# Kernel optimization log

Hardware: AMD Instinct MI355X
Metric: run time of the kernel (lower is better)

Reference implementation:

```python
import jax, jax.numpy as jnp
import numpy as np

N, K, D, H, DK, DV, L, E = 16384, 16, 128, 8, 16, 16, 2, 32
DFF = 4 * D
EPS = 1e-5


def _ln(x, g, b):
    mu = jnp.mean(x, axis=-1, keepdims=True)
    var = jnp.var(x, axis=-1, keepdims=True)
    return (x - mu) * jax.lax.rsqrt(var + EPS) * g + b


def setup_inputs() -> dict:
    key = jax.random.key(0)
    ks = jax.random.split(key, 20)
    inp = {
        "node_h": jax.random.normal(ks[0], (N, D), jnp.float32),
        "src_idx": jax.random.randint(ks[1], (N, K), 0, N),
        "edge_feat": jax.random.normal(ks[2], (N, K, E), jnp.float32),
        "t": jax.random.uniform(ks[3], (N, K), jnp.float32),
        "t_now": jnp.ones((1,), jnp.float32),
        # params (linear weights stored [in, out])
        "edge_fc_w": jax.random.normal(ks[4], (E, D), jnp.float32) * (2.0 / (E + D)) ** 0.5,
        "edge_fc_b": jnp.zeros((D,), jnp.float32),
        "basis_freq": jnp.asarray(1.0 / 10 ** np.linspace(0, 9, D), jnp.float32),
        "phase": jax.random.normal(ks[5], (D,), jnp.float32),
        "wq": jax.random.normal(ks[6], (L, D, H * DK), jnp.float32) * np.sqrt(2.0 / (D + DK)),
        "wk": jax.random.normal(ks[7], (L, D, H * DK), jnp.float32) * np.sqrt(2.0 / (D + DK)),
        "wv": jax.random.normal(ks[8], (L, D, H * DV), jnp.float32) * np.sqrt(2.0 / (D + DV)),
        "attn_fc_w": jax.random.normal(ks[9], (L, H * DV, D), jnp.float32) * (2.0 / (H * DV + D)) ** 0.5,
        "attn_fc_b": jnp.zeros((L, D), jnp.float32),
        "attn_ln_g": jnp.ones((L, D), jnp.float32),
        "attn_ln_b": jnp.zeros((L, D), jnp.float32),
        "ffn_w1": jax.random.normal(ks[10], (L, D, DFF), jnp.float32) * (1.0 / D) ** 0.5,
        "ffn_b1": jnp.zeros((L, DFF), jnp.float32),
        "ffn_w2": jax.random.normal(ks[11], (L, DFF, D), jnp.float32) * (1.0 / DFF) ** 0.5,
        "ffn_b2": jnp.zeros((L, D), jnp.float32),
        "ffn_ln_g": jnp.ones((L, D), jnp.float32),
        "ffn_ln_b": jnp.zeros((L, D), jnp.float32),
        "fea2node_w": jax.random.normal(ks[12], (D, D), jnp.float32) * (2.0 / (D + D)) ** 0.5,
        "fea2node_b": jnp.zeros((D,), jnp.float32),
        "final_ln_g": jnp.ones((D,), jnp.float32),
        "final_ln_b": jnp.zeros((D,), jnp.float32),
    }
    return inp


def reference(node_h, src_idx, edge_feat, t, t_now,
              edge_fc_w, edge_fc_b, basis_freq, phase,
              wq, wk, wv, attn_fc_w, attn_fc_b, attn_ln_g, attn_ln_b,
              ffn_w1, ffn_b1, ffn_w2, ffn_b2, ffn_ln_g, ffn_ln_b,
              fea2node_w, fea2node_b, final_ln_g, final_ln_b):
    scale = 1.0 / np.sqrt(DK).astype(np.float32)
    # message_func: gather src features, edge transform, temporal encoding
    t_enc = jnp.cos((t_now[0] - t)[..., None] * basis_freq + phase)        # [N,K,D]
    z = node_h[src_idx] + jax.nn.gelu(edge_feat @ edge_fc_w + edge_fc_b) + t_enc
    # reduce_func: inner_layer transformer blocks over the K-neighbor mailbox
    f = z
    for i in range(L):
        q = (f @ wq[i]).reshape(N, K, H, DK)
        k = (f @ wk[i]).reshape(N, K, H, DK)
        v = (f @ wv[i]).reshape(N, K, H, DV)
        attn = jax.nn.softmax(jnp.einsum('nqhd,nkhd->nhqk', q, k) * scale, axis=-1)
        out = jnp.einsum('nhqk,nkhd->nqhd', attn, v).reshape(N, K, H * DV)
        f = _ln(out @ attn_fc_w[i] + attn_fc_b[i] + f, attn_ln_g[i], attn_ln_b[i])
        hid = jax.nn.relu(f @ ffn_w1[i] + ffn_b1[i])                        # [N,K,4D]
        f = _ln(hid @ ffn_w2[i] + ffn_b2[i] + f, ffn_ln_g[i], ffn_ln_b[i])
    pooled = jnp.mean(f, axis=1)                                            # [N,D]
    out = _ln(jax.nn.gelu(pooled @ fea2node_w + fea2node_b) + node_h,
              final_ln_g, final_ln_b)
    return out
```

## Files before the change

### kernel.cpp

```cpp
#include <hip/hip_runtime.h>

#define NN 16384
#define OFF_EWT 0
#define OFF_WQT 4096
#define OFF_WKT 36864
#define OFF_WVT 69632
#define OFF_AFT 102400
#define OFF_W1T 135168
#define OFF_W2T 266240
#define OFF_F2N 397312
#define TOTAL_W 413696

typedef __attribute__((ext_vector_type(8))) short bf16x8;
typedef __attribute__((ext_vector_type(4))) short bf16x4;
typedef __attribute__((ext_vector_type(4))) float f32x4;

static __device__ __forceinline__ short f2bf(float f) {
  unsigned u = __builtin_bit_cast(unsigned, f);
  u += 0x7fffu + ((u >> 16) & 1u);
  return (short)(u >> 16);
}
static __device__ __forceinline__ float bf2f(short h) {
  unsigned u = ((unsigned)(unsigned short)h) << 16;
  return __builtin_bit_cast(float, u);
}
static __device__ __forceinline__ float gelu_f(float x) {
  float e = __expf(1.5957691216057308f * (x + 0.044715f * x * x * x));
  return x - x / (e + 1.0f);
}
static __device__ __forceinline__ f32x4 mfma16(bf16x8 a, bf16x8 b, f32x4 c) {
  return __builtin_amdgcn_mfma_f32_16x16x32_bf16(a, b, c, 0, 0, 0);
}
#define SWZM(row) (((((row) & 7) << 4)) ^ ((((row) >> 3) & 3) << 5))
static __device__ __forceinline__ int swzb(int row, int col) {
  return row * 256 + ((col * 2) ^ SWZM(row));
}
static __device__ __forceinline__ bf16x8 tile_ld8(const short* base, int row, int col) {
  return *(const bf16x8*)((const char*)base + swzb(row, col));
}
static __device__ __forceinline__ void tile_st16(short* base, int row, int col, short v) {
  *(short*)((char*)base + swzb(row, col)) = v;
}
static __device__ __forceinline__ void stage_w(short* dst, const short* src, int stride,
                                               int w, int lane) {
  #pragma unroll
  for (int it = 0; it < 4; ++it) {
    int dbase = (it * 4 + w) * 1024;
    int d = dbase + lane * 16;
    int row = d >> 8;
    int scolb = (d & 255) ^ SWZM(row);
    const short* sp = src + row * stride + (scolb >> 1);
    __builtin_amdgcn_global_load_lds(
        (const __attribute__((address_space(1))) unsigned int*)sp,
        (__attribute__((address_space(3))) unsigned int*)((char*)dst + dbase),
        16, 0, 0);
  }
}

#define LDS_FENCE() do {                                       \
    asm volatile("s_waitcnt lgkmcnt(0)" ::: "memory");         \
    __builtin_amdgcn_sched_barrier(0);                         \
  } while (0)

#define ISSUE(SRC, STRIDE) stage_w(bn, (SRC), (STRIDE), w, lane)
#define ENDSTEP() do {                                         \
    __syncthreads();                                           \
    short* _t = bc; bc = bn; bn = _t;                          \
  } while (0)

#define LD_FA(SRC)                                                        \
  _Pragma("unroll") for (int _s = 0; _s < 4; ++_s)                        \
      fA[_s] = tile_ld8((SRC), li, _s * 32 + lq * 8);

#define ST_TILE(T, ACC)                                                   \
  _Pragma("unroll") for (int _c = 0; _c < 8; ++_c)                        \
    _Pragma("unroll") for (int _r = 0; _r < 4; ++_r)                      \
      tile_st16((T), lq * 4 + _r, _c * 16 + li, f2bf((ACC)[_c][_r]));

#define PROJ4(AR, BB)                                                     \
    f32x4 g0 = F0, g1 = F0, g2 = F0, g3 = F0;                             \
    _Pragma("unroll") for (int _s = 0; _s < 4; ++_s) {                    \
      int _sc = _s * 32 + lq * 8;                                         \
      g0 = mfma16(AR[_s], tile_ld8((BB), 0 + li, _sc), g0);               \
      g1 = mfma16(AR[_s], tile_ld8((BB), 16 + li, _sc), g1);              \
      g2 = mfma16(AR[_s], tile_ld8((BB), 32 + li, _sc), g2);              \
      g3 = mfma16(AR[_s], tile_ld8((BB), 48 + li, _sc), g3);              \
    }

#define ST4(DST, CB)                                                      \
    _Pragma("unroll") for (int _r = 0; _r < 4; ++_r) {                    \
      tile_st16((DST), lq * 4 + _r, ((CB) + 0) * 16 + li, f2bf(g0[_r])); \
      tile_st16((DST), lq * 4 + _r, ((CB) + 1) * 16 + li, f2bf(g1[_r])); \
      tile_st16((DST), lq * 4 + _r, ((CB) + 2) * 16 + li, f2bf(g2[_r])); \
      tile_st16((DST), lq * 4 + _r, ((CB) + 3) * 16 + li, f2bf(g3[_r])); \
    }

#define ACC4(AR, CB, BB)                                                  \
    _Pragma("unroll") for (int _s = 0; _s < 4; ++_s) {                    \
      int _sc = _s * 32 + lq * 8;                                         \
      acc[(CB) + 0] = mfma16(AR[_s], tile_ld8((BB), 0 + li, _sc), acc[(CB) + 0]);  \
      acc[(CB) + 1] = mfma16(AR[_s], tile_ld8((BB), 16 + li, _sc), acc[(CB) + 1]); \
      acc[(CB) + 2] = mfma16(AR[_s], tile_ld8((BB), 32 + li, _sc), acc[(CB) + 2]); \
      acc[(CB) + 3] = mfma16(AR[_s], tile_ld8((BB), 48 + li, _sc), acc[(CB) + 3]); \
    }

#define LAYER_NORM(A, GP, BP) do {                                        \
    float _gg[8], _bb[8];                                                 \
    _Pragma("unroll") for (int _c = 0; _c < 8; ++_c) {                    \
      _gg[_c] = (GP)[_c * 16 + li]; _bb[_c] = (BP)[_c * 16 + li]; }       \
    _Pragma("unroll") for (int _r = 0; _r < 4; ++_r) {                    \
      float _s1 = 0.f, _s2 = 0.f;                                         \
      _Pragma("unroll") for (int _c = 0; _c < 8; ++_c) {                  \
        float _v = (A)[_c][_r]; _s1 += _v; _s2 += _v * _v; }              \
      _Pragma("unroll") for (int _m = 1; _m <= 8; _m <<= 1) {             \
        _s1 += __shfl_xor(_s1, _m, 64); _s2 += __shfl_xor(_s2, _m, 64); } \
      float _mean = _s1 * (1.f / 128.f);                                  \
      float _var = _s2 * (1.f / 128.f) - _mean * _mean;                   \
      float _rstd = rsqrtf(_var + 1e-5f);                                 \
      _Pragma("unroll") for (int _c = 0; _c < 8; ++_c)                    \
        (A)[_c][_r] = ((A)[_c][_r] - _mean) * _rstd * _gg[_c] + _bb[_c];  \
    }                                                                     \
  } while (0)

__global__ void prep_kernel(const float* __restrict__ ew, const float* __restrict__ wq,
                            const float* __restrict__ wk, const float* __restrict__ wv,
                            const float* __restrict__ afc, const float* __restrict__ w1,
                            const float* __restrict__ w2, const float* __restrict__ f2n,
                            short* __restrict__ wsb) {
  int tt = blockIdx.x * 256 + threadIdx.x;
  if (tt >= TOTAL_W) return;
  short v;
  if (tt < OFF_WQT) {
    int u = tt; int row = u >> 5, colr = u & 31;
    v = f2bf(ew[colr * 128 + row]);
  } else if (tt < OFF_WKT) {
    int u = tt - OFF_WQT; int i = u >> 14; u &= 16383; int row = u >> 7, colr = u & 127;
    v = f2bf(wq[i * 16384 + colr * 128 + row]);
  } else if (tt < OFF_WVT) {
    int u = tt - OFF_WKT; int i = u >> 14; u &= 16383; int row = u >> 7, colr = u & 127;
    v = f2bf(wk[i * 16384 + colr * 128 + row]);
  } else if (tt < OFF_AFT) {
    int u = tt - OFF_WVT; int i = u >> 14; u &= 16383; int row = u >> 7, colr = u & 127;
    v = f2bf(wv[i * 16384 + colr * 128 + row]);
  } else if (tt < OFF_W1T) {
    int u = tt - OFF_AFT; int i = u >> 14; u &= 16383; int row = u >> 7, colr = u & 127;
    v = f2bf(afc[i * 16384 + colr * 128 + row]);
  } else if (tt < OFF_W2T) {
    int u = tt - OFF_W1T; int i = u >> 16; u &= 65535; int row = u >> 7, colr = u & 127;
    v = f2bf(w1[i * 65536 + colr * 512 + row]);
  } else if (tt < OFF_F2N) {
    int u = tt - OFF_W2T; int i = u >> 16; u &= 65535; int row = u >> 9, colr = u & 511;
    v = f2bf(w2[i * 65536 + colr * 128 + row]);
  } else {
    int u = tt - OFF_F2N; int row = u >> 7, colr = u & 127;
    v = f2bf(f2n[colr * 128 + row]);
  }
  wsb[tt] = v;
}

__global__ __launch_bounds__(256, 2) void fused_kernel(
    const float* __restrict__ node_h, const int* __restrict__ src_idx,
    const float* __restrict__ edge_feat, const float* __restrict__ t_arr,
    const float* __restrict__ t_now, const float* __restrict__ edge_fc_b,
    const float* __restrict__ basis_freq, const float* __restrict__ phase,
    const float* __restrict__ attn_fc_b, const float* __restrict__ attn_ln_g,
    const float* __restrict__ attn_ln_b, const float* __restrict__ ffn_b1,
    const float* __restrict__ ffn_b2, const float* __restrict__ ffn_ln_g,
    const float* __restrict__ ffn_ln_b, const float* __restrict__ f2n_b,
    const float* __restrict__ fin_g, const float* __restrict__ fin_b,
    const short* __restrict__ wsb, float* __restrict__ out) {
  __shared__ __align__(16) short bufs0[8192];
  __shared__ __align__(16) short bufs1[8192];
  __shared__ __align__(16) short lds_qk[4][4096];

  const int tid = (int)threadIdx.x;
  const int w = tid >> 6, lane = tid & 63, li = lane & 15, lq = lane >> 4;
  const int n = (int)blockIdx.x * 4 + w;
  short* myQ = lds_qk[w];
  short* myK = lds_qk[w] + 2048;
  short* bc = bufs0;
  short* bn = bufs1;
  const f32x4 F0 = {0.f, 0.f, 0.f, 0.f};
  const bf16x8 B0 = {0, 0, 0, 0, 0, 0, 0, 0};

  stage_w(bc, wsb + OFF_WQT, 128, w, lane);

  const float tnow = t_now[0];

  f32x4 acc[8];
  {
    const float* ef = edge_feat + ((size_t)(n * 16 + li)) * 32 + lq * 8;
    f32x4 e0 = *(const f32x4*)(ef);
    f32x4 e1 = *(const f32x4*)(ef + 4);
    bf16x8 ea;
    #pragma unroll
    for (int j = 0; j < 4; ++j) { ea[j] = f2bf(e0[j]); ea[j + 4] = f2bf(e1[j]); }
    const short* ewt = wsb + OFF_EWT;
    #pragma unroll
    for (int c = 0; c < 8; ++c) {
      bf16x8 eb = *(const bf16x8*)(ewt + (c * 16 + li) * 32 + lq * 8);
      acc[c] = mfma16(ea, eb, F0);
    }
  }
  {
    float bfq[8], phs[8], ebs[8];
    #pragma unroll
    for (int c = 0; c < 8; ++c) {
      int col = c * 16 + li;
      bfq[c] = basis_freq[col]; phs[c] = phase[col]; ebs[c] = edge_fc_b[col];
    }
    #pragma unroll
    for (int r = 0; r < 4; ++r) {
      int m = lq * 4 + r;
      int sidx = src_idx[n * 16 + m];
      float dt = tnow - t_arr[n * 16 + m];
      const float* nh = node_h + (size_t)sidx * 128;
      #pragma unroll
      for (int c = 0; c < 8; ++c) {
        int col = c * 16 + li;
        float x = gelu_f(acc[c][r] + ebs[c]);
        x += nh[col];
        x += __cosf(dt * bfq[c] + phs[c]);
        acc[c][r] = x;
      }
    }
  }
  ST_TILE(myQ, acc);
  __syncthreads();

  bf16x8 fA[4];

  for (int il = 0; il < 2; ++il) {
    const short* WQT = wsb + OFF_WQT + il * 16384;
    const short* WKT = wsb + OFF_WKT + il * 16384;
    const short* WVT = wsb + OFF_WVT + il * 16384;
    const short* AFT = wsb + OFF_AFT + il * 16384;
    const short* W1T = wsb + OFF_W1T + il * 65536;
    const short* W2T = wsb + OFF_W2T + il * 65536;
    const short* WQN = wsb + OFF_WQT + ((il == 0) ? 16384 : 0);

    ISSUE(WQT + 8192, 128);
    LD_FA(myQ);
    { PROJ4(fA, bc); ST4(myQ, 0); }
    ENDSTEP();
    ISSUE(WKT, 128);
    { PROJ4(fA, bc); ST4(myQ, 4); }
    ENDSTEP();
    ISSUE(WKT + 8192, 128);
    { PROJ4(fA, bc); ST4(myK, 0); }
    ENDSTEP();
    ISSUE(WVT, 128);
    { PROJ4(fA, bc); ST4(myK, 4); }
    ENDSTEP();
    f32x4 vacc[8];
    ISSUE(WVT + 8192, 128);
    { PROJ4(fA, bc); vacc[0] = g0; vacc[1] = g1; vacc[2] = g2; vacc[3] = g3; }
    ENDSTEP();
    ISSUE(AFT, 128);
    { PROJ4(fA, bc); vacc[4] = g0; vacc[5] = g1; vacc[6] = g2; vacc[7] = g3; }
    {
      f32x4 st[8];
      #pragma unroll
      for (int h = 0; h < 8; ++h) {
        bf16x8 ka = B0, qa = B0;
        if (lq < 2) {
          ka = tile_ld8(myK, li, h * 16 + lq * 8);
          qa = tile_ld8(myQ, li, h * 16 + lq * 8);
        }
        st[h] = mfma16(ka, qa, F0);
      }
      LDS_FENCE();
      #pragma unroll
      for (int c = 0; c < 8; ++c) {
        bf16x4 pkv;
        #pragma unroll
        for (int r = 0; r < 4; ++r) pkv[r] = f2bf(vacc[c][r]);
        *(bf16x4*)(myK + (c * 16 + li) * 16 + lq * 4) = pkv;
      }
      LDS_FENCE();
      #pragma unroll
      for (int h = 0; h < 8; ++h) {
        float p[4]; float mx = -1e30f;
        #pragma unroll
        for (int r = 0; r < 4; ++r) { p[r] = st[h][r] * 0.25f; mx = fmaxf(mx, p[r]); }
        mx = fmaxf(mx, __shfl_xor(mx, 16, 64));
        mx = fmaxf(mx, __shfl_xor(mx, 32, 64));
        float sum = 0.f;
        #pragma unroll
        for (int r = 0; r < 4; ++r) { p[r] = __expf(p[r] - mx); sum += p[r]; }
        sum += __shfl_xor(sum, 16, 64);
        sum += __shfl_xor(sum, 32, 64);
        float inv = 1.0f / sum;
        #pragma unroll
        for (int r = 0; r < 4; ++r) p[r] *= inv;
        bf16x8 pa;
        #pragma unroll
        for (int j = 0; j < 8; ++j) {
          float v = __shfl(p[j & 3], li + 16 * (2 * lq + (j >> 2)), 64);
          pa[j] = (lq < 2) ? f2bf(v) : (short)0;
        }
        bf16x8 vb = B0;
        if (lq < 2) vb = *(const bf16x8*)(myK + (h * 16 + li) * 16 + lq * 8);
        f32x4 o = mfma16(pa, vb, F0);
        #pragma unroll
        for (int r = 0; r < 4; ++r)
          tile_st16(myQ, lq * 4 + r, h * 16 + li, f2bf(o[r]));
      }
      LDS_FENCE();
    }
    bf16x8 oa[4];
    #pragma unroll
    for (int s = 0; s < 4; ++s) oa[s] = tile_ld8(myQ, li, s * 32 + lq * 8);
    ENDSTEP();
    ISSUE(AFT + 8192, 128);
    #pragma unroll
    for (int j = 0; j < 4; ++j) {
      float b = attn_fc_b[il * 128 + j * 16 + li];
      #pragma unroll
      for (int r = 0; r < 4; ++r) acc[j][r] += b;
    }
    ACC4(oa, 0, bc);
    ENDSTEP();
    ISSUE(W1T, 128);
    #pragma unroll
    for (int j = 0; j < 4; ++j) {
      float b = attn_fc_b[il * 128 + (4 + j) * 16 + li];
      #pragma unroll
      for (int r = 0; r < 4; ++r) acc[4 + j][r] += b;
    }
    ACC4(oa, 4, bc);
    LAYER_NORM(acc, attn_ln_g + il * 128, attn_ln_b + il * 128);
    ST_TILE(myQ, acc);
    LD_FA(myQ);
    #pragma unroll
    for (int c = 0; c < 8; ++c) {
      float b2 = ffn_b2[il * 128 + c * 16 + li];
      #pragma unroll
      for (int r = 0; r < 4; ++r) acc[c][r] += b2;
    }
    ENDSTEP();

    for (int ct = 0; ct < 4; ++ct) {
      const short* W1c = W1T + ct * 16384;
      const short* W2c = W2T + ct * 128;
      const float* b1p = ffn_b1 + il * 512 + ct * 128;
      ISSUE(W1c + 8192, 128);
      {
        PROJ4(fA, bc);
        float b10 = b1p[0 * 16 + li], b11 = b1p[1 * 16 + li];
        float b12 = b1p[2 * 16 + li], b13 = b1p[3 * 16 + li];
        #pragma unroll
        for (int r = 0; r < 4; ++r) {
          tile_st16(myK, lq * 4 + r, 0 * 16 + li, f2bf(fmaxf(g0[r] + b10, 0.f)));
          tile_st16(myK, lq * 4 + r, 1 * 16 + li, f2bf(fmaxf(g1[r] + b11, 0.f)));
          tile_st16(myK, lq * 4 + r, 2 * 16 + li, f2bf(fmaxf(g2[r] + b12, 0.f)));
          tile_st16(myK, lq * 4 + r, 3 * 16 + li, f2bf(fmaxf(g3[r] + b13, 0.f)));
        }
      }
      ENDSTEP();
      ISSUE(W2c, 512);
      {
        PROJ4(fA, bc);
        float b14 = b1p[4 * 16 + li], b15 = b1p[5 * 16 + li];
        float b16 = b1p[6 * 16 + li], b17 = b1p[7 * 16 + li];
        #pragma unroll
        for (int r = 0; r < 4; ++r) {
          tile_st16(myK, lq * 4 + r, 4 * 16 + li, f2bf(fmaxf(g0[r] + b14, 0.f)));
          tile_st16(myK, lq * 4 + r, 5 * 16 + li, f2bf(fmaxf(g1[r] + b15, 0.f)));
          tile_st16(myK, lq * 4 + r, 6 * 16 + li, f2bf(fmaxf(g2[r] + b16, 0.f)));
          tile_st16(myK, lq * 4 + r, 7 * 16 + li, f2bf(fmaxf(g3[r] + b17, 0.f)));
        }
      }
      LDS_FENCE();
      bf16x8 ha[4];
      #pragma unroll
      for (int s = 0; s < 4; ++s) ha[s] = tile_ld8(myK, li, s * 32 + lq * 8);
      ENDSTEP();
      ISSUE(W2c + 64 * 512, 512);
      ACC4(ha, 0, bc);
      ENDSTEP();
      {
        const short* nx = (ct < 3) ? (W1T + (ct + 1) * 16384) : WQN;
        ISSUE(nx, 128);
      }
      ACC4(ha, 4, bc);
      if (ct == 3) {
        LAYER_NORM(acc, ffn_ln_g + il * 128, ffn_ln_b + il * 128);
        ST_TILE(myQ, acc);
      }
      ENDSTEP();
    }
  }

  float pc[8];
  #pragma unroll
  for (int c = 0; c < 8; ++c) {
    float s = acc[c][0] + acc[c][1] + acc[c][2] + acc[c][3];
    s += __shfl_xor(s, 16, 64);
    s += __shfl_xor(s, 32, 64);
    pc[c] = s * (1.f / 16.f);
  }
  float* ps = (float*)myK;
  if (lq == 0) {
    #pragma unroll
    for (int c = 0; c < 8; ++c) ps[c * 16 + li] = pc[c];
  }
  LDS_FENCE();
  const short* F2NT = wsb + OFF_F2N;
  float yv[2];
  #pragma unroll
  for (int half = 0; half < 2; ++half) {
    int col = half * 64 + lane;
    float dot = 0.f;
    for (int d0 = 0; d0 < 128; d0 += 8) {
      bf16x8 wv8 = *(const bf16x8*)(F2NT + col * 128 + d0);
      f32x4 p0 = *(const f32x4*)(ps + d0);
      f32x4 p1 = *(const f32x4*)(ps + d0 + 4);
      dot += p0[0] * bf2f(wv8[0]) + p0[1] * bf2f(wv8[1]) + p0[2] * bf2f(wv8[2]) + p0[3] * bf2f(wv8[3]);
      dot += p1[0] * bf2f(wv8[4]) + p1[1] * bf2f(wv8[5]) + p1[2] * bf2f(wv8[6]) + p1[3] * bf2f(wv8[7]);
    }
    yv[half] = gelu_f(dot + f2n_b[col]) + node_h[(size_t)n * 128 + col];
  }
  float s1 = yv[0] + yv[1], s2 = yv[0] * yv[0] + yv[1] * yv[1];
  #pragma unroll
  for (int m = 1; m <= 32; m <<= 1) { s1 += __shfl_xor(s1, m, 64); s2 += __shfl_xor(s2, m, 64); }
  float mean = s1 * (1.f / 128.f);
  float var = s2 * (1.f / 128.f) - mean * mean;
  float rstd = rsqrtf(var + 1e-5f);
  #pragma unroll
  for (int half = 0; half < 2; ++half) {
    int col = half * 64 + lane;
    out[(size_t)n * 128 + col] = (yv[half] - mean) * rstd * fin_g[col] + fin_b[col];
  }
}

extern "C" void kernel_launch(void* const* d_in, const int* in_sizes, int n_in,
                              void* d_out, int out_size, void* d_ws, size_t ws_size,
                              hipStream_t stream) {
  const float* node_h    = (const float*)d_in[0];
  const int*   src_idx   = (const int*)d_in[1];
  const float* edge_feat = (const float*)d_in[2];
  const float* t_arr     = (const float*)d_in[3];
  const float* t_now     = (const float*)d_in[4];
  const float* edge_fc_w = (const float*)d_in[5];
  const float* edge_fc_b = (const float*)d_in[6];
  const float* basis_frq = (const float*)d_in[7];
  const float* phase     = (const float*)d_in[8];
  const float* wq        = (const float*)d_in[9];
  const float* wk        = (const float*)d_in[10];
  const float* wv        = (const float*)d_in[11];
  const float* attn_fc_w = (const float*)d_in[12];
  const float* attn_fc_b = (const float*)d_in[13];
  const float* attn_ln_g = (const float*)d_in[14];
  const float* attn_ln_b = (const float*)d_in[15];
  const float* ffn_w1    = (const float*)d_in[16];
  const float* ffn_b1    = (const float*)d_in[17];
  const float* ffn_w2    = (const float*)d_in[18];
  const float* ffn_b2    = (const float*)d_in[19];
  const float* ffn_ln_g  = (const float*)d_in[20];
  const float* ffn_ln_b  = (const float*)d_in[21];
  const float* f2n_w     = (const float*)d_in[22];
  const float* f2n_b     = (const float*)d_in[23];
  const float* fin_g     = (const float*)d_in[24];
  const float* fin_b     = (const float*)d_in[25];
  short* wsb = (short*)d_ws;

  prep_kernel<<<(TOTAL_W + 255) / 256, 256, 0, stream>>>(
      edge_fc_w, wq, wk, wv, attn_fc_w, ffn_w1, ffn_w2, f2n_w, wsb);
  fused_kernel<<<NN / 4, 256, 0, stream>>>(
      node_h, src_idx, edge_feat, t_arr, t_now, edge_fc_b, basis_frq, phase,
      attn_fc_b, attn_ln_g, attn_ln_b, ffn_b1, ffn_b2, ffn_ln_g, ffn_ln_b,
      f2n_b, fin_g, fin_b, wsb, (float*)d_out);
}
```

Baseline: 758.2 us.

## Process two nodes per wavefront to reuse staged weight tiles across both

```diff
diff --git a/kernel.cpp b/kernel.cpp
--- a/kernel.cpp
+++ b/kernel.cpp
@@ -44,7 +44,7 @@
 static __device__ __forceinline__ void stage_w(short* dst, const short* src, int stride,
                                                int w, int lane) {
   #pragma unroll
-  for (int it = 0; it < 4; ++it) {
+  for (int it = 0; it < 2; ++it) {
     int dbase = (it * 4 + w) * 1024;
     int d = dbase + lane * 16;
     int row = d >> 8;
@@ -68,40 +68,45 @@
     short* _t = bc; bc = bn; bn = _t;                          \
   } while (0)
 
-#define LD_FA(SRC)                                                        \
-  _Pragma("unroll") for (int _s = 0; _s < 4; ++_s)                        \
-      fA[_s] = tile_ld8((SRC), li, _s * 32 + lq * 8);
+#define LD_FA2() do {                                                     \
+    _Pragma("unroll") for (int _s = 0; _s < 4; ++_s) {                    \
+      fA0[_s] = tile_ld8(myQ0, li, _s * 32 + lq * 8);                     \
+      fA1[_s] = tile_ld8(myQ1, li, _s * 32 + lq * 8);                     \
+    }                                                                     \
+  } while (0)
 
 #define ST_TILE(T, ACC)                                                   \
   _Pragma("unroll") for (int _c = 0; _c < 8; ++_c)                        \
     _Pragma("unroll") for (int _r = 0; _r < 4; ++_r)                      \
       tile_st16((T), lq * 4 + _r, _c * 16 + li, f2bf((ACC)[_c][_r]));
 
-#define PROJ4(AR, BB)                                                     \
-    f32x4 g0 = F0, g1 = F0, g2 = F0, g3 = F0;                             \
+#define PROJ2D(BB)                                                        \
+    f32x4 ga0 = F0, ga1 = F0, gb0 = F0, gb1 = F0;                         \
     _Pragma("unroll") for (int _s = 0; _s < 4; ++_s) {                    \
       int _sc = _s * 32 + lq * 8;                                         \
-      g0 = mfma16(AR[_s], tile_ld8((BB), 0 + li, _sc), g0);               \
-      g1 = mfma16(AR[_s], tile_ld8((BB), 16 + li, _sc), g1);              \
-      g2 = mfma16(AR[_s], tile_ld8((BB), 32 + li, _sc), g2);              \
-      g3 = mfma16(AR[_s], tile_ld8((BB), 48 + li, _sc), g3);              \
-    }
-
-#define ST4(DST, CB)                                                      \
+      bf16x8 _b0 = tile_ld8((BB), 0 + li, _sc);                           \
+      bf16x8 _b1 = tile_ld8((BB), 16 + li, _sc);                          \
+      ga0 = mfma16(fA0[_s], _b0, ga0); gb0 = mfma16(fA1[_s], _b0, gb0);   \
+      ga1 = mfma16(fA0[_s], _b1, ga1); gb1 = mfma16(fA1[_s], _b1, gb1);   \
+    }
+
+#define ST2D(D0, D1, CB)                                                  \
     _Pragma("unroll") for (int _r = 0; _r < 4; ++_r) {                    \
-      tile_st16((DST), lq * 4 + _r, ((CB) + 0) * 16 + li, f2bf(g0[_r])); \
-      tile_st16((DST), lq * 4 + _r, ((CB) + 1) * 16 + li, f2bf(g1[_r])); \
-      tile_st16((DST), lq * 4 + _r, ((CB) + 2) * 16 + li, f2bf(g2[_r])); \
-      tile_st16((DST), lq * 4 + _r, ((CB) + 3) * 16 + li, f2bf(g3[_r])); \
-    }
-
-#define ACC4(AR, CB, BB)                                                  \
+      tile_st16((D0), lq * 4 + _r, (CB) * 16 + li, f2bf(ga0[_r]));        \
+      tile_st16((D0), lq * 4 + _r, ((CB) + 1) * 16 + li, f2bf(ga1[_r]));  \
+      tile_st16((D1), lq * 4 + _r, (CB) * 16 + li, f2bf(gb0[_r]));        \
+      tile_st16((D1), lq * 4 + _r, ((CB) + 1) * 16 + li, f2bf(gb1[_r]));  \
+    }
+
+#define ACC2D(AR0, AR1, CB, BB)                                           \
     _Pragma("unroll") for (int _s = 0; _s < 4; ++_s) {                    \
       int _sc = _s * 32 + lq * 8;                                         \
-      acc[(CB) + 0] = mfma16(AR[_s], tile_ld8((BB), 0 + li, _sc), acc[(CB) + 0]);  \
-      acc[(CB) + 1] = mfma16(AR[_s], tile_ld8((BB), 16 + li, _sc), acc[(CB) + 1]); \
-      acc[(CB) + 2] = mfma16(AR[_s], tile_ld8((BB), 32 + li, _sc), acc[(CB) + 2]); \
-      acc[(CB) + 3] = mfma16(AR[_s], tile_ld8((BB), 48 + li, _sc), acc[(CB) + 3]); \
+      bf16x8 _b0 = tile_ld8((BB), 0 + li, _sc);                           \
+      bf16x8 _b1 = tile_ld8((BB), 16 + li, _sc);                          \
+      acc0[(CB)] = mfma16(AR0[_s], _b0, acc0[(CB)]);                      \
+      acc1[(CB)] = mfma16(AR1[_s], _b0, acc1[(CB)]);                      \
+      acc0[(CB) + 1] = mfma16(AR0[_s], _b1, acc0[(CB) + 1]);              \
+      acc1[(CB) + 1] = mfma16(AR1[_s], _b1, acc1[(CB) + 1]);              \
     }
 
 #define LAYER_NORM(A, GP, BP) do {                                        \
@@ -120,6 +125,53 @@
       _Pragma("unroll") for (int _c = 0; _c < 8; ++_c)                    \
         (A)[_c][_r] = ((A)[_c][_r] - _mean) * _rstd * _gg[_c] + _bb[_c];  \
     }                                                                     \
+  } while (0)
+
+#define ATTN(MYQ, MYK, VACC, OA) do {                                     \
+    f32x4 _st[8];                                                         \
+    _Pragma("unroll") for (int _h = 0; _h < 8; ++_h) {                    \
+      bf16x8 _ka = B0, _qa = B0;                                          \
+      if (lq < 2) {                                                       \
+        _ka = tile_ld8((MYK), li, _h * 16 + lq * 8);                      \
+        _qa = tile_ld8((MYQ), li, _h * 16 + lq * 8);                      \
+      }                                                                   \
+      _st[_h] = mfma16(_ka, _qa, F0);                                     \
+    }                                                                     \
+    LDS_FENCE();                                                          \
+    _Pragma("unroll") for (int _c = 0; _c < 8; ++_c) {                    \
+      bf16x4 _pk;                                                         \
+      _Pragma("unroll") for (int _r = 0; _r < 4; ++_r)                    \
+        _pk[_r] = f2bf((VACC)[_c][_r]);                                   \
+      *(bf16x4*)((MYK) + (_c * 16 + li) * 16 + lq * 4) = _pk;             \
+    }                                                                     \
+    LDS_FENCE();                                                          \
+    _Pragma("unroll") for (int _h = 0; _h < 8; ++_h) {                    \
+      float _p[4]; float _mx = -1e30f;                                    \
+      _Pragma("unroll") for (int _r = 0; _r < 4; ++_r) {                  \
+        _p[_r] = _st[_h][_r] * 0.25f; _mx = fmaxf(_mx, _p[_r]); }         \
+      _mx = fmaxf(_mx, __shfl_xor(_mx, 16, 64));                          \
+      _mx = fmaxf(_mx, __shfl_xor(_mx, 32, 64));                          \
+      float _sum = 0.f;                                                   \
+      _Pragma("unroll") for (int _r = 0; _r < 4; ++_r) {                  \
+        _p[_r] = __expf(_p[_r] - _mx); _sum += _p[_r]; }                  \
+      _sum += __shfl_xor(_sum, 16, 64);                                   \
+      _sum += __shfl_xor(_sum, 32, 64);                                   \
+      float _inv = 1.0f / _sum;                                           \
+      _Pragma("unroll") for (int _r = 0; _r < 4; ++_r) _p[_r] *= _inv;    \
+      bf16x8 _pa;                                                         \
+      _Pragma("unroll") for (int _j = 0; _j < 8; ++_j) {                  \
+        float _v = __shfl(_p[_j & 3], li + 16 * (2 * lq + (_j >> 2)), 64);\
+        _pa[_j] = (lq < 2) ? f2bf(_v) : (short)0;                         \
+      }                                                                   \
+      bf16x8 _vb = B0;                                                    \
+      if (lq < 2) _vb = *(const bf16x8*)((MYK) + (_h * 16 + li) * 16 + lq * 8); \
+      f32x4 _o = mfma16(_pa, _vb, F0);                                    \
+      _Pragma("unroll") for (int _r = 0; _r < 4; ++_r)                    \
+        tile_st16((MYQ), lq * 4 + _r, _h * 16 + li, f2bf(_o[_r]));        \
+    }                                                                     \
+    LDS_FENCE();                                                          \
+    _Pragma("unroll") for (int _s = 0; _s < 4; ++_s)                      \
+      (OA)[_s] = tile_ld8((MYQ), li, _s * 32 + lq * 8);                   \
   } while (0)
 
 __global__ void prep_kernel(const float* __restrict__ ew, const float* __restrict__ wq,
@@ -169,15 +221,18 @@
     const float* __restrict__ ffn_ln_b, const float* __restrict__ f2n_b,
     const float* __restrict__ fin_g, const float* __restrict__ fin_b,
     const short* __restrict__ wsb, float* __restrict__ out) {
-  __shared__ __align__(16) short bufs0[8192];
-  __shared__ __align__(16) short bufs1[8192];
-  __shared__ __align__(16) short lds_qk[4][4096];
+  __shared__ __align__(16) short bufs0[4096];
+  __shared__ __align__(16) short bufs1[4096];
+  __shared__ __align__(16) short lds_qk[4][8192];
 
   const int tid = (int)threadIdx.x;
   const int w = tid >> 6, lane = tid & 63, li = lane & 15, lq = lane >> 4;
-  const int n = (int)blockIdx.x * 4 + w;
-  short* myQ = lds_qk[w];
-  short* myK = lds_qk[w] + 2048;
+  const int n0 = (int)blockIdx.x * 8 + w * 2;
+  const int n1 = n0 + 1;
+  short* myQ0 = lds_qk[w];
+  short* myK0 = lds_qk[w] + 2048;
+  short* myQ1 = lds_qk[w] + 4096;
+  short* myK1 = lds_qk[w] + 6144;
   short* bc = bufs0;
   short* bn = bufs1;
   const f32x4 F0 = {0.f, 0.f, 0.f, 0.f};
@@ -187,19 +242,24 @@
 
   const float tnow = t_now[0];
 
-  f32x4 acc[8];
+  f32x4 acc0[8], acc1[8];
   {
-    const float* ef = edge_feat + ((size_t)(n * 16 + li)) * 32 + lq * 8;
-    f32x4 e0 = *(const f32x4*)(ef);
-    f32x4 e1 = *(const f32x4*)(ef + 4);
-    bf16x8 ea;
-    #pragma unroll
-    for (int j = 0; j < 4; ++j) { ea[j] = f2bf(e0[j]); ea[j + 4] = f2bf(e1[j]); }
     const short* ewt = wsb + OFF_EWT;
+    const float* ef0 = edge_feat + ((size_t)(n0 * 16 + li)) * 32 + lq * 8;
+    const float* ef1 = edge_feat + ((size_t)(n1 * 16 + li)) * 32 + lq * 8;
+    f32x4 ea0 = *(const f32x4*)(ef0), ea0b = *(const f32x4*)(ef0 + 4);
+    f32x4 ea1 = *(const f32x4*)(ef1), ea1b = *(const f32x4*)(ef1 + 4);
+    bf16x8 e0, e1;
+    #pragma unroll
+    for (int j = 0; j < 4; ++j) {
+      e0[j] = f2bf(ea0[j]); e0[j + 4] = f2bf(ea0b[j]);
+      e1[j] = f2bf(ea1[j]); e1[j + 4] = f2bf(ea1b[j]);
+    }
     #pragma unroll
     for (int c = 0; c < 8; ++c) {
       bf16x8 eb = *(const bf16x8*)(ewt + (c * 16 + li) * 32 + lq * 8);
-      acc[c] = mfma16(ea, eb, F0);
+      acc0[c] = mfma16(e0, eb, F0);
+      acc1[c] = mfma16(e1, eb, F0);
     }
   }
   {
@@ -212,23 +272,25 @@
     #pragma unroll
     for (int r = 0; r < 4; ++r) {
       int m = lq * 4 + r;
-      int sidx = src_idx[n * 16 + m];
-      float dt = tnow - t_arr[n * 16 + m];
-      const float* nh = node_h + (size_t)sidx * 128;
+      int s0 = src_idx[n0 * 16 + m], s1 = src_idx[n1 * 16 + m];
+      float dt0 = tnow - t_arr[n0 * 16 + m], dt1 = tnow - t_arr[n1 * 16 + m];
+      const float* nh0 = node_h + (size_t)s0 * 128;
+      const float* nh1 = node_h + (size_t)s1 * 128;
       #pragma unroll
       for (int c = 0; c < 8; ++c) {
         int col = c * 16 + li;
-        float x = gelu_f(acc[c][r] + ebs[c]);
-        x += nh[col];
-        x += __cosf(dt * bfq[c] + phs[c]);
-        acc[c][r] = x;
+        acc0[c][r] = gelu_f(acc0[c][r] + ebs[c]) + nh0[col] + __cosf(dt0 * bfq[c] + phs[c]);
+        acc1[c][r] = gelu_f(acc1[c][r] + ebs[c]) + nh1[col] + __cosf(dt1 * bfq[c] + phs[c]);
       }
     }
   }
-  ST_TILE(myQ, acc);
+  ST_TILE(myQ0, acc0);
+  ST_TILE(myQ1, acc1);
   __syncthreads();
 
-  bf16x8 fA[4];
+  bf16x8 fA0[4], fA1[4];
+  bf16x8 oa0_[4], oa1_[4];
+  bf16x8 ha0_[4], ha1_[4];
 
   for (int il = 0; il < 2; ++il) {
     const short* WQT = wsb + OFF_WQT + il * 16384;
@@ -239,198 +301,166 @@
     const short* W2T = wsb + OFF_W2T + il * 65536;
     const short* WQN = wsb + OFF_WQT + ((il == 0) ? 16384 : 0);
 
-    ISSUE(WQT + 8192, 128);
-    LD_FA(myQ);
-    { PROJ4(fA, bc); ST4(myQ, 0); }
-    ENDSTEP();
-    ISSUE(WKT, 128);
-    { PROJ4(fA, bc); ST4(myQ, 4); }
-    ENDSTEP();
-    ISSUE(WKT + 8192, 128);
-    { PROJ4(fA, bc); ST4(myK, 0); }
-    ENDSTEP();
-    ISSUE(WVT, 128);
-    { PROJ4(fA, bc); ST4(myK, 4); }
-    ENDSTEP();
-    f32x4 vacc[8];
-    ISSUE(WVT + 8192, 128);
-    { PROJ4(fA, bc); vacc[0] = g0; vacc[1] = g1; vacc[2] = g2; vacc[3] = g3; }
-    ENDSTEP();
-    ISSUE(AFT, 128);
-    { PROJ4(fA, bc); vacc[4] = g0; vacc[5] = g1; vacc[6] = g2; vacc[7] = g3; }
-    {
-      f32x4 st[8];
-      #pragma unroll
-      for (int h = 0; h < 8; ++h) {
-        bf16x8 ka = B0, qa = B0;
-        if (lq < 2) {
-          ka = tile_ld8(myK, li, h * 16 + lq * 8);
-          qa = tile_ld8(myQ, li, h * 16 + lq * 8);
+    f32x4 vacc0[8], vacc1[8];
+
+    #pragma unroll
+    for (int q = 0; q < 4; ++q) {
+      const short* nx = (q < 3) ? (WQT + (q + 1) * 4096) : WKT;
+      ISSUE(nx, 128);
+      if (q == 0) LD_FA2();
+      { PROJ2D(bc); ST2D(myQ0, myQ1, q * 2); }
+      ENDSTEP();
+    }
+    #pragma unroll
+    for (int q = 0; q < 4; ++q) {
+      const short* nx = (q < 3) ? (WKT + (q + 1) * 4096) : WVT;
+      ISSUE(nx, 128);
+      { PROJ2D(bc); ST2D(myK0, myK1, q * 2); }
+      ENDSTEP();
+    }
+    #pragma unroll
+    for (int q = 0; q < 4; ++q) {
+      const short* nx = (q < 3) ? (WVT + (q + 1) * 4096) : AFT;
+      ISSUE(nx, 128);
+      {
+        PROJ2D(bc);
+        vacc0[q * 2] = ga0; vacc0[q * 2 + 1] = ga1;
+        vacc1[q * 2] = gb0; vacc1[q * 2 + 1] = gb1;
+      }
+      if (q == 3) {
+        ATTN(myQ0, myK0, vacc0, oa0_);
+        ATTN(myQ1, myK1, vacc1, oa1_);
+      }
+      ENDSTEP();
+    }
+    #pragma unroll
+    for (int q = 0; q < 4; ++q) {
+      const short* nx = (q < 3) ? (AFT + (q + 1) * 4096) : W1T;
+      ISSUE(nx, 128);
+      #pragma unroll
+      for (int j = 0; j < 2; ++j) {
+        float b = attn_fc_b[il * 128 + (q * 2 + j) * 16 + li];
+        #pragma unroll
+        for (int r = 0; r < 4; ++r) { acc0[q * 2 + j][r] += b; acc1[q * 2 + j][r] += b; }
+      }
+      ACC2D(oa0_, oa1_, q * 2, bc);
+      if (q == 3) {
+        LAYER_NORM(acc0, attn_ln_g + il * 128, attn_ln_b + il * 128);
+        LAYER_NORM(acc1, attn_ln_g + il * 128, attn_ln_b + il * 128);
+        ST_TILE(myQ0, acc0);
+        ST_TILE(myQ1, acc1);
+        LD_FA2();
+        #pragma unroll
+        for (int c = 0; c < 8; ++c) {
+          float b2 = ffn_b2[il * 128 + c * 16 + li];
+          #pragma unroll
+          for (int r = 0; r < 4; ++r) { acc0[c][r] += b2; acc1[c][r] += b2; }
         }
-        st[h] = mfma16(ka, qa, F0);
-      }
-      LDS_FENCE();
-      #pragma unroll
-      for (int c = 0; c < 8; ++c) {
-        bf16x4 pkv;
-        #pragma unroll
-        for (int r = 0; r < 4; ++r) pkv[r] = f2bf(vacc[c][r]);
-        *(bf16x4*)(myK + (c * 16 + li) * 16 + lq * 4) = pkv;
-      }
-      LDS_FENCE();
-      #pragma unroll
-      for (int h = 0; h < 8; ++h) {
-        float p[4]; float mx = -1e30f;
-        #pragma unroll
-        for (int r = 0; r < 4; ++r) { p[r] = st[h][r] * 0.25f; mx = fmaxf(mx, p[r]); }
-        mx = fmaxf(mx, __shfl_xor(mx, 16, 64));
-        mx = fmaxf(mx, __shfl_xor(mx, 32, 64));
-        float sum = 0.f;
-        #pragma unroll
-        for (int r = 0; r < 4; ++r) { p[r] = __expf(p[r] - mx); sum += p[r]; }
-        sum += __shfl_xor(sum, 16, 64);
-        sum += __shfl_xor(sum, 32, 64);
-        float inv = 1.0f / sum;
-        #pragma unroll
-        for (int r = 0; r < 4; ++r) p[r] *= inv;
-        bf16x8 pa;
-        #pragma unroll
-        for (int j = 0; j < 8; ++j) {
-          float v = __shfl(p[j & 3], li + 16 * (2 * lq + (j >> 2)), 64);
-          pa[j] = (lq < 2) ? f2bf(v) : (short)0;
-        }
-        bf16x8 vb = B0;
-        if (lq < 2) vb = *(const bf16x8*)(myK + (h * 16 + li) * 16 + lq * 8);
-        f32x4 o = mfma16(pa, vb, F0);
-        #pragma unroll
-        for (int r = 0; r < 4; ++r)
-          tile_st16(myQ, lq * 4 + r, h * 16 + li, f2bf(o[r]));
-      }
-      LDS_FENCE();
-    }
-    bf16x8 oa[4];
-    #pragma unroll
-    for (int s = 0; s < 4; ++s) oa[s] = tile_ld8(myQ, li, s * 32 + lq * 8);
-    ENDSTEP();
-    ISSUE(AFT + 8192, 128);
-    #pragma unroll
-    for (int j = 0; j < 4; ++j) {
-      float b = attn_fc_b[il * 128 + j * 16 + li];
-      #pragma unroll
-      for (int r = 0; r < 4; ++r) acc[j][r] += b;
-    }
-    ACC4(oa, 0, bc);
-    ENDSTEP();
-    ISSUE(W1T, 128);
-    #pragma unroll
-    for (int j = 0; j < 4; ++j) {
-      float b = attn_fc_b[il * 128 + (4 + j) * 16 + li];
-      #pragma unroll
-      for (int r = 0; r < 4; ++r) acc[4 + j][r] += b;
-    }
-    ACC4(oa, 4, bc);
-    LAYER_NORM(acc, attn_ln_g + il * 128, attn_ln_b + il * 128);
-    ST_TILE(myQ, acc);
-    LD_FA(myQ);
-    #pragma unroll
-    for (int c = 0; c < 8; ++c) {
-      float b2 = ffn_b2[il * 128 + c * 16 + li];
-      #pragma unroll
-      for (int r = 0; r < 4; ++r) acc[c][r] += b2;
-    }
-    ENDSTEP();
+      }
+      ENDSTEP();
+    }
 
     for (int ct = 0; ct < 4; ++ct) {
       const short* W1c = W1T + ct * 16384;
       const short* W2c = W2T + ct * 128;
       const float* b1p = ffn_b1 + il * 512 + ct * 128;
-      ISSUE(W1c + 8192, 128);
-      {
-        PROJ4(fA, bc);
-        float b10 = b1p[0 * 16 + li], b11 = b1p[1 * 16 + li];
-        float b12 = b1p[2 * 16 + li], b13 = b1p[3 * 16 + li];
-        #pragma unroll
-        for (int r = 0; r < 4; ++r) {
-          tile_st16(myK, lq * 4 + r, 0 * 16 + li, f2bf(fmaxf(g0[r] + b10, 0.f)));
-          tile_st16(myK, lq * 4 + r, 1 * 16 + li, f2bf(fmaxf(g1[r] + b11, 0.f)));
-          tile_st16(myK, lq * 4 + r, 2 * 16 + li, f2bf(fmaxf(g2[r] + b12, 0.f)));
-          tile_st16(myK, lq * 4 + r, 3 * 16 + li, f2bf(fmaxf(g3[r] + b13, 0.f)));
+      #pragma unroll
+      for (int q = 0; q < 4; ++q) {
+        const short* nx = (q < 3) ? (W1c + (q + 1) * 4096) : W2c;
+        ISSUE(nx, (q < 3) ? 128 : 512);
+        {
+          PROJ2D(bc);
+          float ba = b1p[(q * 2) * 16 + li], bb = b1p[(q * 2 + 1) * 16 + li];
+          #pragma unroll
+          for (int r = 0; r < 4; ++r) {
+            tile_st16(myK0, lq * 4 + r, (q * 2) * 16 + li, f2bf(fmaxf(ga0[r] + ba, 0.f)));
+            tile_st16(myK0, lq * 4 + r, (q * 2 + 1) * 16 + li, f2bf(fmaxf(ga1[r] + bb, 0.f)));
+            tile_st16(myK1, lq * 4 + r, (q * 2) * 16 + li, f2bf(fmaxf(gb0[r] + ba, 0.f)));
+            tile_st16(myK1, lq * 4 + r, (q * 2 + 1) * 16 + li, f2bf(fmaxf(gb1[r] + bb, 0.f)));
+          }
         }
-      }
-      ENDSTEP();
-      ISSUE(W2c, 512);
-      {
-        PROJ4(fA, bc);
-        float b14 = b1p[4 * 16 + li], b15 = b1p[5 * 16 + li];
-        float b16 = b1p[6 * 16 + li], b17 = b1p[7 * 16 + li];
-        #pragma unroll
-        for (int r = 0; r < 4; ++r) {
-          tile_st16(myK, lq * 4 + r, 4 * 16 + li, f2bf(fmaxf(g0[r] + b14, 0.f)));
-          tile_st16(myK, lq * 4 + r, 5 * 16 + li, f2bf(fmaxf(g1[r] + b15, 0.f)));
-          tile_st16(myK, lq * 4 + r, 6 * 16 + li, f2bf(fmaxf(g2[r] + b16, 0.f)));
-          tile_st16(myK, lq * 4 + r, 7 * 16 + li, f2bf(fmaxf(g3[r] + b17, 0.f)));
+        if (q == 3) {
+          LDS_FENCE();
+          #pragma unroll
+          for (int s = 0; s < 4; ++s) {
+            ha0_[s] = tile_ld8(myK0, li, s * 32 + lq * 8);
+            ha1_[s] = tile_ld8(myK1, li, s * 32 + lq * 8);
+          }
         }
-      }
-      LDS_FENCE();
-      bf16x8 ha[4];
-      #pragma unroll
-      for (int s = 0; s < 4; ++s) ha[s] = tile_ld8(myK, li, s * 32 + lq * 8);
-      ENDSTEP();
-      ISSUE(W2c + 64 * 512, 512);
-      ACC4(ha, 0, bc);
-      ENDSTEP();
-      {
-        const short* nx = (ct < 3) ? (W1T + (ct + 1) * 16384) : WQN;
-        ISSUE(nx, 128);
-      }
-      ACC4(ha, 4, bc);
-      if (ct == 3) {
-        LAYER_NORM(acc, ffn_ln_g + il * 128, ffn_ln_b + il * 128);
-        ST_TILE(myQ, acc);
-      }
-      ENDSTEP();
+        ENDSTEP();
+      }
+      #pragma unroll
+      for (int q = 0; q < 4; ++q) {
+        const short* nx;
+        int nstr;
+        if (q < 3) { nx = W2c + (q + 1) * 32 * 512; nstr = 512; }
+        else if (ct < 3) { nx = W1T + (ct + 1) * 16384; nstr = 128; }
+        else { nx = WQN; nstr = 128; }
+        ISSUE(nx, nstr);
+        ACC2D(ha0_, ha1_, q * 2, bc);
+        if (ct == 3 && q == 3) {
+          LAYER_NORM(acc0, ffn_ln_g + il * 128, ffn_ln_b + il * 128);
+          LAYER_NORM(acc1, ffn_ln_g + il * 128, ffn_ln_b + il * 128);
+          ST_TILE(myQ0, acc0);
+          ST_TILE(myQ1, acc1);
+        }
+        ENDSTEP();
+      }
     }
   }
-
-  float pc[8];
-  #pragma unroll
-  for (int c = 0; c < 8; ++c) {
-    float s = acc[c][0] + acc[c][1] + acc[c][2] + acc[c][3];
-    s += __shfl_xor(s, 16, 64);
-    s += __shfl_xor(s, 32, 64);
-    pc[c] = s * (1.f / 16.f);
-  }
-  float* ps = (float*)myK;
-  if (lq == 0) {
-    #pragma unroll
-    for (int c = 0; c < 8; ++c) ps[c * 16 + li] = pc[c];
-  }
-  LDS_FENCE();
-  const short* F2NT = wsb + OFF_F2N;
-  float yv[2];
-  #pragma unroll
-  for (int half = 0; half < 2; ++half) {
-    int col = half * 64 + lane;
-    float dot = 0.f;
-    for (int d0 = 0; d0 < 128; d0 += 8) {
-      bf16x8 wv8 = *(const bf16x8*)(F2NT + col * 128 + d0);
-      f32x4 p0 = *(const f32x4*)(ps + d0);
-      f32x4 p1 = *(const f32x4*)(ps + d0 + 4);
-      dot += p0[0] * bf2f(wv8[0]) + p0[1] * bf2f(wv8[1]) + p0[2] * bf2f(wv8[2]) + p0[3] * bf2f(wv8[3]);
-      dot += p1[0] * bf2f(wv8[4]) + p1[1] * bf2f(wv8[5]) + p1[2] * bf2f(wv8[6]) + p1[3] * bf2f(wv8[7]);
-    }
-    yv[half] = gelu_f(dot + f2n_b[col]) + node_h[(size_t)n * 128 + col];
-  }
-  float s1 = yv[0] + yv[1], s2 = yv[0] * yv[0] + yv[1] * yv[1];
-  #pragma unroll
-  for (int m = 1; m <= 32; m <<= 1) { s1 += __shfl_xor(s1, m, 64); s2 += __shfl_xor(s2, m, 64); }
-  float mean = s1 * (1.f / 128.f);
-  float var = s2 * (1.f / 128.f) - mean * mean;
-  float rstd = rsqrtf(var + 1e-5f);
-  #pragma unroll
-  for (int half = 0; half < 2; ++half) {
-    int col = half * 64 + lane;
-    out[(size_t)n * 128 + col] = (yv[half] - mean) * rstd * fin_g[col] + fin_b[col];
+  asm volatile("s_waitcnt vmcnt(0)" ::: "memory");
+
+  {
+    float pc0[8], pc1[8];
+    #pragma unroll
+    for (int c = 0; c < 8; ++c) {
+      float s0 = acc0[c][0] + acc0[c][1] + acc0[c][2] + acc0[c][3];
+      float s1 = acc1[c][0] + acc1[c][1] + acc1[c][2] + acc1[c][3];
+      s0 += __shfl_xor(s0, 16, 64); s0 += __shfl_xor(s0, 32, 64);
+      s1 += __shfl_xor(s1, 16, 64); s1 += __shfl_xor(s1, 32, 64);
+      pc0[c] = s0 * (1.f / 16.f);
+      pc1[c] = s1 * (1.f / 16.f);
+    }
+    float* ps0 = (float*)myK0;
+    float* ps1 = (float*)myK1;
+    if (lq == 0) {
+      #pragma unroll
+      for (int c = 0; c < 8; ++c) { ps0[c * 16 + li] = pc0[c]; ps1[c * 16 + li] = pc1[c]; }
+    }
+    LDS_FENCE();
+    const short* F2NT = wsb + OFF_F2N;
+    #pragma unroll
+    for (int nd = 0; nd < 2; ++nd) {
+      const float* ps = nd ? ps1 : ps0;
+      int n = nd ? n1 : n0;
+      float yv[2];
+      #pragma unroll
+      for (int half = 0; half < 2; ++half) {
+        int col = half * 64 + lane;
+        float dot = 0.f;
+        for (int d0 = 0; d0 < 128; d0 += 8) {
+          bf16x8 wv8 = *(const bf16x8*)(F2NT + col * 128 + d0);
+          f32x4 p0 = *(const f32x4*)(ps + d0);
+          f32x4 p1 = *(const f32x4*)(ps + d0 + 4);
+          dot += p0[0] * bf2f(wv8[0]) + p0[1] * bf2f(wv8[1]) + p0[2] * bf2f(wv8[2]) + p0[3] * bf2f(wv8[3]);
+          dot += p1[0] * bf2f(wv8[4]) + p1[1] * bf2f(wv8[5]) + p1[2] * bf2f(wv8[6]) + p1[3] * bf2f(wv8[7]);
+        }
+        yv[half] = gelu_f(dot + f2n_b[col]) + node_h[(size_t)n * 128 + col];
+      }
+      float s1v = yv[0] + yv[1], s2v = yv[0] * yv[0] + yv[1] * yv[1];
+      #pragma unroll
+      for (int m = 1; m <= 32; m <<= 1) {
+        s1v += __shfl_xor(s1v, m, 64); s2v += __shfl_xor(s2v, m, 64);
+      }
+      float mean = s1v * (1.f / 128.f);
+      float var = s2v * (1.f / 128.f) - mean * mean;
+      float rstd = rsqrtf(var + 1e-5f);
+      #pragma unroll
+      for (int half = 0; half < 2; ++half) {
+        int col = half * 64 + lane;
+        out[(size_t)n * 128 + col] = (yv[half] - mean) * rstd * fin_g[col] + fin_b[col];
+      }
+    }
   }
 }
 
@@ -467,7 +497,7 @@
 
   prep_kernel<<<(TOTAL_W + 255) / 256, 256, 0, stream>>>(
       edge_fc_w, wq, wk, wv, attn_fc_w, ffn_w1, ffn_w2, f2n_w, wsb);
-  fused_kernel<<<NN / 4, 256, 0, stream>>>(
+  fused_kernel<<<NN / 8, 256, 0, stream>>>(
       node_h, src_idx, edge_feat, t_arr, t_now, edge_fc_b, basis_frq, phase,
       attn_fc_b, attn_ln_g, attn_ln_b, ffn_b1, ffn_b2, ffn_ln_g, ffn_ln_b,
       f2n_b, fin_g, fin_b, wsb, (float*)d_out);
```

Result: faster. 689.7 us (-9.0%).
